# Kernel tuning notes

Hardware: AMD Instinct MI355X
Metric: run time of the kernel (lower is better)

## Reference

```python
import jax, jax.numpy as jnp
import numpy as np

B, N, F_IN, OUT_DIM, H = 8, 2048, 128, 256, 4
D = OUT_DIM // H  # head dim = 64
NEG_SLOPE = 0.2


def setup_inputs() -> dict:
    key = jax.random.key(0)
    k_a, k_x, k_w, k_s, k_d = jax.random.split(key, 5)
    A = jax.random.randint(k_a, (B, N, N), 0, 2).astype(jnp.float32)
    # ensure self-loops so no softmax row is fully masked (-inf -> NaN)
    eye = jnp.eye(N, dtype=jnp.float32)
    A = jnp.maximum(A, eye[None, :, :])
    X = jax.random.normal(k_x, (B, N, F_IN), dtype=jnp.float32)
    # xavier-uniform-like scales
    w_lim = float(np.sqrt(6.0 / (F_IN + OUT_DIM)))
    a_lim = float(np.sqrt(6.0 / (H + D)))
    W = jax.random.uniform(k_w, (OUT_DIM, F_IN), minval=-w_lim, maxval=w_lim, dtype=jnp.float32)
    a_src = jax.random.uniform(k_s, (H, D), minval=-a_lim, maxval=a_lim, dtype=jnp.float32)
    a_dst = jax.random.uniform(k_d, (H, D), minval=-a_lim, maxval=a_lim, dtype=jnp.float32)
    return {"A": A, "X": X, "W": W, "a_src": a_src, "a_dst": a_dst}


def reference(A, X, W, a_src, a_dst):
    b, n, _ = X.shape
    h, d = a_src.shape
    # X_trans = W(X); torch Linear: X @ W.T, W: (out_dim, in_dim)
    X_split = (X @ W.T).reshape(b, n, h, d)  # (b, n, h, d)
    attn_src = jnp.einsum('bnhd,hd->bnh', X_split, a_src)
    attn_dst = jnp.einsum('bnhd,hd->bnh', X_split, a_dst)
    # (b, n, n, h) dense score tensor
    attn = attn_src[:, :, None, :] + attn_dst[:, None, :, :]
    attn = jnp.where(attn >= 0, attn, NEG_SLOPE * attn)  # leaky_relu(0.2)
    attn = jnp.where(A[..., None] == 0, -jnp.inf, attn)
    attn = jax.nn.softmax(attn, axis=2)
    # torch.einsum('bnnk,bnkd->bnkd') with repeated 'n' -> DIAGONAL of attn,
    # elementwise-scaled features (faithful to original code).
    diag = jnp.einsum('bnnh->bnh', attn)  # (b, n, h): self-attention weights
    out = (diag[..., None] * X_split).reshape(b, n, h * d)
    return out
```

## Files before the change

### kernel.cpp

```cpp
#include <hip/hip_runtime.h>
#include <hip/hip_bf16.h>

#define B_   8
#define N_   2048
#define FIN  128
#define OUTD 256
#define H_   4
#define LOG2E 1.44269504088896340736f

typedef __bf16 bf16x8 __attribute__((ext_vector_type(8)));
typedef float  f32x4  __attribute__((ext_vector_type(4)));

__device__ inline __bf16 cvt1(float f) {
    __hip_bfloat16 b = __float2bfloat16(f);
    return *reinterpret_cast<__bf16*>(&b);
}

__global__ __launch_bounds__(256) void gemm_st(const float* __restrict__ X,
                                               const float* __restrict__ W,
                                               const float* __restrict__ a_src,
                                               const float* __restrict__ a_dst,
                                               float* __restrict__ Xt,
                                               float* __restrict__ s_arr,
                                               float* __restrict__ t_arr) {
    int r0   = blockIdx.x * 16;
    int h    = threadIdx.x >> 6;
    int lane = threadIdx.x & 63;
    int m = lane & 15, q = lane >> 4;

    const float* Arow = X + (size_t)(r0 + m) * FIN + q * 8;
    f32x4 acc[4] = {{0,0,0,0},{0,0,0,0},{0,0,0,0},{0,0,0,0}};

#pragma unroll
    for (int kc = 0; kc < 4; ++kc) {
        float4 alo = *(const float4*)(Arow + kc * 32);
        float4 ahi = *(const float4*)(Arow + kc * 32 + 4);
        bf16x8 af;
        af[0] = cvt1(alo.x); af[1] = cvt1(alo.y); af[2] = cvt1(alo.z); af[3] = cvt1(alo.w);
        af[4] = cvt1(ahi.x); af[5] = cvt1(ahi.y); af[6] = cvt1(ahi.z); af[7] = cvt1(ahi.w);
#pragma unroll
        for (int ct = 0; ct < 4; ++ct) {
            const float* Wrow = W + (size_t)(h * 64 + ct * 16 + m) * FIN + q * 8 + kc * 32;
            float4 blo = *(const float4*)(Wrow);
            float4 bhi = *(const float4*)(Wrow + 4);
            bf16x8 bf;
            bf[0] = cvt1(blo.x); bf[1] = cvt1(blo.y); bf[2] = cvt1(blo.z); bf[3] = cvt1(blo.w);
            bf[4] = cvt1(bhi.x); bf[5] = cvt1(bhi.y); bf[6] = cvt1(bhi.z); bf[7] = cvt1(bhi.w);
            acc[ct] = __builtin_amdgcn_mfma_f32_16x16x32_bf16(af, bf, acc[ct], 0, 0, 0);
        }
    }

#pragma unroll
    for (int ct = 0; ct < 4; ++ct) {
        float* outp = Xt + (size_t)(r0 + q * 4) * OUTD + h * 64 + ct * 16 + m;
#pragma unroll
        for (int reg = 0; reg < 4; ++reg)
            outp[(size_t)reg * OUTD] = acc[ct][reg];
    }

    float sp[4] = {0, 0, 0, 0}, tp[4] = {0, 0, 0, 0};
#pragma unroll
    for (int ct = 0; ct < 4; ++ct) {
        float as = a_src[h * 64 + ct * 16 + m];
        float ad = a_dst[h * 64 + ct * 16 + m];
#pragma unroll
        for (int reg = 0; reg < 4; ++reg) {
            sp[reg] = fmaf(acc[ct][reg], as, sp[reg]);
            tp[reg] = fmaf(acc[ct][reg], ad, tp[reg]);
        }
    }
#pragma unroll
    for (int off = 1; off < 16; off <<= 1) {
#pragma unroll
        for (int reg = 0; reg < 4; ++reg) {
            sp[reg] += __shfl_xor(sp[reg], off);
            tp[reg] += __shfl_xor(tp[reg], off);
        }
    }
    if (m == 0) {
#pragma unroll
        for (int reg = 0; reg < 4; ++reg) {
            size_t row = (size_t)(r0 + q * 4 + reg);
            s_arr[row * H_ + h] = sp[reg] * LOG2E;
            t_arr[row * H_ + h] = tp[reg] * LOG2E;
        }
    }
}

__global__ __launch_bounds__(256) void gat_main(const float* __restrict__ A,
                                                const float* __restrict__ s_arr,
                                                const float* __restrict__ t_arr,
                                                float* __restrict__ out) {
    __shared__ float t_lds[N_ * H_];
    __shared__ float diag_lds[16][H_];

    int b  = blockIdx.x >> 7;
    int rt = blockIdx.x & 127;
    int r0 = rt * 16;
    int tid = threadIdx.x;

    {
        const float4* tsrc = (const float4*)(t_arr + (size_t)b * N_ * H_);
        float4* tdst = (float4*)t_lds;
#pragma unroll
        for (int i = 0; i < (N_ * H_) / 4 / 256; ++i)
            tdst[tid + i * 256] = tsrc[tid + i * 256];
    }
    __syncthreads();

    int r  = tid >> 4;
    int lj = tid & 15;
    int gi = r0 + r;

    f32x4 s4 = *(const f32x4*)(s_arr + ((size_t)b * N_ + gi) * H_);
    const float* Arow = A + ((size_t)b * N_ + gi) * N_;

    f32x4 acc = {0.f, 0.f, 0.f, 0.f};

    auto body = [&](float4 a4, int it) {
        int j = it * 64 + lj * 4;
#pragma unroll
        for (int jj = 0; jj < 4; ++jj) {
            f32x4 t4 = ((const f32x4*)t_lds)[j + jj];
            float aj = (jj == 0) ? a4.x : (jj == 1) ? a4.y : (jj == 2) ? a4.z : a4.w;
#pragma unroll
            for (int hh = 0; hh < H_; ++hh) {
                float y = s4[hh] + t4[hh];
                y = fmaxf(y, 0.2f * y);
                acc[hh] = fmaf(aj, __builtin_amdgcn_exp2f(y), acc[hh]);
            }
        }
    };

    float4 a4 = *(const float4*)(Arow + lj * 4);
    for (int it = 0; it < 31; ++it) {
        float4 a4n = *(const float4*)(Arow + (it + 1) * 64 + lj * 4);
        body(a4, it);
        a4 = a4n;
    }
    body(a4, 31);

#pragma unroll
    for (int mk = 8; mk > 0; mk >>= 1) {
        acc[0] += __shfl_xor(acc[0], mk);
        acc[1] += __shfl_xor(acc[1], mk);
        acc[2] += __shfl_xor(acc[2], mk);
        acc[3] += __shfl_xor(acc[3], mk);
    }
    if (lj == 0) {
        f32x4 ti = ((const f32x4*)t_lds)[gi];
#pragma unroll
        for (int hh = 0; hh < H_; ++hh) {
            float y = s4[hh] + ti[hh];
            y = fmaxf(y, 0.2f * y);
            diag_lds[r][hh] = __builtin_amdgcn_exp2f(y) / acc[hh];
        }
    }
    __syncthreads();

    float* orow = out + ((size_t)b * N_ + gi) * OUTD;
#pragma unroll
    for (int ii = 0; ii < 4; ++ii) {
        int c = lj * 4 + ii * 64;
        float4 v = *(float4*)(orow + c);
        float dg = diag_lds[r][ii];
        v.x *= dg; v.y *= dg; v.z *= dg; v.w *= dg;
        *(float4*)(orow + c) = v;
    }
}

extern "C" void kernel_launch(void* const* d_in, const int* in_sizes, int n_in,
                              void* d_out, int out_size, void* d_ws, size_t ws_size,
                              hipStream_t stream) {
    const float* A     = (const float*)d_in[0];
    const float* X     = (const float*)d_in[1];
    const float* W     = (const float*)d_in[2];
    const float* a_src = (const float*)d_in[3];
    const float* a_dst = (const float*)d_in[4];
    float* out = (float*)d_out;

    char* ws = (char*)d_ws;
    float* s_arr = (float*)ws;
    float* t_arr = (float*)(ws + 262144);

    gemm_st<<<1024, 256, 0, stream>>>(X, W, a_src, a_dst, out, s_arr, t_arr);
    gat_main<<<1024, 256, 0, stream>>>(A, s_arr, t_arr, out);
}
```

Baseline: 234.1 us.

## Drop LDS staging of t vector, read from global, deepen A prefetch

```diff
diff --git a/kernel.cpp b/kernel.cpp
--- a/kernel.cpp
+++ b/kernel.cpp
@@ -87,33 +87,20 @@
     }
 }
 
-__global__ __launch_bounds__(256) void gat_main(const float* __restrict__ A,
-                                                const float* __restrict__ s_arr,
-                                                const float* __restrict__ t_arr,
-                                                float* __restrict__ out) {
-    __shared__ float t_lds[N_ * H_];
-    __shared__ float diag_lds[16][H_];
+__global__ __launch_bounds__(256, 8) void gat_main(const float* __restrict__ A,
+                                                   const float* __restrict__ s_arr,
+                                                   const float* __restrict__ t_arr,
+                                                   float* __restrict__ out) {
+    int b   = blockIdx.x >> 7;
+    int rt  = blockIdx.x & 127;
+    int tid = threadIdx.x;
+    int r   = tid >> 4;
+    int lj  = tid & 15;
+    int gi  = rt * 16 + r;
 
-    int b  = blockIdx.x >> 7;
-    int rt = blockIdx.x & 127;
-    int r0 = rt * 16;
-    int tid = threadIdx.x;
-
-    {
-        const float4* tsrc = (const float4*)(t_arr + (size_t)b * N_ * H_);
-        float4* tdst = (float4*)t_lds;
-#pragma unroll
-        for (int i = 0; i < (N_ * H_) / 4 / 256; ++i)
-            tdst[tid + i * 256] = tsrc[tid + i * 256];
-    }
-    __syncthreads();
-
-    int r  = tid >> 4;
-    int lj = tid & 15;
-    int gi = r0 + r;
-
+    const f32x4* __restrict__ trow = (const f32x4*)(t_arr + (size_t)b * N_ * H_);
     f32x4 s4 = *(const f32x4*)(s_arr + ((size_t)b * N_ + gi) * H_);
-    const float* Arow = A + ((size_t)b * N_ + gi) * N_;
+    const float* __restrict__ Arow = A + ((size_t)b * N_ + gi) * N_;
 
     f32x4 acc = {0.f, 0.f, 0.f, 0.f};
 
@@ -121,7 +108,7 @@
         int j = it * 64 + lj * 4;
 #pragma unroll
         for (int jj = 0; jj < 4; ++jj) {
-            f32x4 t4 = ((const f32x4*)t_lds)[j + jj];
+            f32x4 t4 = trow[j + jj];
             float aj = (jj == 0) ? a4.x : (jj == 1) ? a4.y : (jj == 2) ? a4.z : a4.w;
 #pragma unroll
             for (int hh = 0; hh < H_; ++hh) {
@@ -132,13 +119,15 @@
         }
     };
 
-    float4 a4 = *(const float4*)(Arow + lj * 4);
-    for (int it = 0; it < 31; ++it) {
-        float4 a4n = *(const float4*)(Arow + (it + 1) * 64 + lj * 4);
-        body(a4, it);
-        a4 = a4n;
+    float4 a0 = *(const float4*)(Arow + lj * 4);
+    float4 a1 = *(const float4*)(Arow + 64 + lj * 4);
+    for (int it = 0; it < 30; ++it) {
+        float4 an = *(const float4*)(Arow + (it + 2) * 64 + lj * 4);
+        body(a0, it);
+        a0 = a1; a1 = an;
     }
-    body(a4, 31);
+    body(a0, 30);
+    body(a1, 31);
 
 #pragma unroll
     for (int mk = 8; mk > 0; mk >>= 1) {
@@ -147,24 +136,23 @@
         acc[2] += __shfl_xor(acc[2], mk);
         acc[3] += __shfl_xor(acc[3], mk);
     }
-    if (lj == 0) {
-        f32x4 ti = ((const f32x4*)t_lds)[gi];
+
+    f32x4 ti = trow[gi];
+    f32x4 dg;
 #pragma unroll
-        for (int hh = 0; hh < H_; ++hh) {
-            float y = s4[hh] + ti[hh];
-            y = fmaxf(y, 0.2f * y);
-            diag_lds[r][hh] = __builtin_amdgcn_exp2f(y) / acc[hh];
-        }
+    for (int hh = 0; hh < H_; ++hh) {
+        float y = s4[hh] + ti[hh];
+        y = fmaxf(y, 0.2f * y);
+        dg[hh] = __builtin_amdgcn_exp2f(y) / acc[hh];
     }
-    __syncthreads();
 
     float* orow = out + ((size_t)b * N_ + gi) * OUTD;
 #pragma unroll
     for (int ii = 0; ii < 4; ++ii) {
         int c = lj * 4 + ii * 64;
         float4 v = *(float4*)(orow + c);
-        float dg = diag_lds[r][ii];
-        v.x *= dg; v.y *= dg; v.z *= dg; v.w *= dg;
+        float d = dg[ii];
+        v.x *= d; v.y *= d; v.z *= d; v.w *= d;
         *(float4*)(orow + c) = v;
     }
 }
```

After: 238.1 us. No clear change (+1.7%).
